# Kernel optimization log

Measured on AMD Instinct MI355X. Metric: run time of the kernel, lower is better.

## Reference

```python
import jax, jax.numpy as jnp
import numpy as np

B, S, D, H = 2, 2048, 1024, 16
HD = D // H
NEG = -1000000.0


def setup_inputs() -> dict:
    key = jax.random.key(0)
    ks = jax.random.split(key, 8)
    sc = 1.0 / np.sqrt(D)
    return {
        "q": jax.random.normal(ks[0], (B, S, D), dtype=jnp.float32),
        "k": jax.random.normal(ks[1], (B, S, D), dtype=jnp.float32),
        "v": jax.random.normal(ks[2], (B, S, D), dtype=jnp.float32),
        "valid_lens": jax.random.randint(ks[3], (B,), 1, S + 1, dtype=jnp.int32),
        "Wq": jax.random.normal(ks[4], (D, D), dtype=jnp.float32) * sc,
        "Wk": jax.random.normal(ks[5], (D, D), dtype=jnp.float32) * sc,
        "Wv": jax.random.normal(ks[6], (D, D), dtype=jnp.float32) * sc,
        "Wo": jax.random.normal(ks[7], (D, D), dtype=jnp.float32) * sc,
    }


def reference(q, k, v, valid_lens, Wq, Wk, Wv, Wo):
    # projections: [B,S,D] -> [B,H,S,HD]
    def split_heads(x):
        return x.reshape(B, S, H, HD).transpose(0, 2, 1, 3)

    qh = split_heads(q @ Wq)
    kh = split_heads(k @ Wk)
    vh = split_heads(v @ Wv)

    # scaled dot-product scores: [B,H,Sq,Sk]
    scores = jnp.einsum("bhqd,bhkd->bhqk", qh, kh) / jnp.sqrt(
        jnp.asarray(HD, dtype=jnp.float32))

    # sequence mask over key axis: positions >= valid_len replaced by -1e6
    key_pos = jnp.arange(S, dtype=jnp.int32)
    mask = key_pos[None, :] < valid_lens[:, None]            # [B,Sk]
    scores = jnp.where(mask[:, None, None, :], scores, NEG)

    attn = jax.nn.softmax(scores, axis=-1)                   # dropout rate 0
    ctx = jnp.einsum("bhqk,bhkd->bhqd", attn, vh)            # [B,H,S,HD]
    out = ctx.transpose(0, 2, 1, 3).reshape(B, S, D)
    return out @ Wo
```

## Files before the change

### kernel.cpp

```cpp
#include <hip/hip_runtime.h>
#include <math.h>

#define NB 2
#define NS 2048
#define ND 1024
#define NH 16
#define NHD 64
#define GK 1024
#define NEG -1000000.0f

typedef __attribute__((ext_vector_type(4))) float f32x4;
typedef __attribute__((ext_vector_type(8))) _Float16 f16x8;
typedef __attribute__((ext_vector_type(4))) _Float16 f16x4;

typedef const __attribute__((address_space(1))) unsigned int* gas_t;
typedef __attribute__((address_space(3))) unsigned int* las_t;

__global__ __launch_bounds__(256) void wt_kernel(const float* __restrict__ Wq,
                                                 const float* __restrict__ Wk,
                                                 const float* __restrict__ Wv,
                                                 const float* __restrict__ Wo,
                                                 _Float16* __restrict__ WtBase) {
  __shared__ _Float16 Ts[64][72];
  const int which = blockIdx.x >> 8;
  const int rem = blockIdx.x & 255;
  const int tk = rem >> 4;
  const int tn = rem & 15;
  const float* W = which == 0 ? Wq : which == 1 ? Wk : which == 2 ? Wv : Wo;
  _Float16* Wt = WtBase + (size_t)which * (GK * ND);
  const int t = threadIdx.x;
#pragma unroll
  for (int p = 0; p < 4; ++p) {
    const int kr = (p << 4) + (t >> 4);
    const int nc = (t & 15) << 2;
    float4 v = *(const float4*)(W + (size_t)((tk << 6) + kr) * ND + (tn << 6) + nc);
    f16x4 h = {(_Float16)v.x, (_Float16)v.y, (_Float16)v.z, (_Float16)v.w};
    *(f16x4*)&Ts[kr][nc] = h;
  }
  __syncthreads();
#pragma unroll
  for (int p = 0; p < 4; ++p) {
    const int nr = (p << 4) + (t >> 4);
    const int kc = (t & 15) << 2;
    f16x4 h;
#pragma unroll
    for (int u = 0; u < 4; ++u) h[u] = Ts[kc + u][nr];
    *(f16x4*)(Wt + (size_t)((tn << 6) + nr) * GK + (tk << 6) + kc) = h;
  }
}

template<int AMODE, int OMODE, int BN>
__global__ __launch_bounds__(256) void gemm_kernel(const void* __restrict__ Ap0,
                                                   const void* __restrict__ Ap1,
                                                   const void* __restrict__ Ap2,
                                                   const _Float16* __restrict__ BtBase,
                                                   void* __restrict__ OutBase) {
  constexpr int BM = 128, BK = 32;
  constexpr int NBN = ND / BN;
  constexpr int BLKS = (NB * NS / BM) * NBN;
  constexpr int NF = BN / 32;
  __shared__ float    As32[AMODE == 0 ? BM * BK : 8];
  __shared__ _Float16 As16[AMODE == 1 ? BM * BK : 8];
  __shared__ _Float16 Bs[BN * BK];

  int idx = blockIdx.x;
  const int which = idx / BLKS;
  idx -= which * BLKS;
  const int bm = (idx / NBN) * BM;
  const int bn = (idx % NBN) * BN;
  const void* Ap = which == 0 ? Ap0 : which == 1 ? Ap1 : Ap2;
  const _Float16* Bt = BtBase + (size_t)which * (ND * GK);

  const int tid = threadIdx.x, lane = tid & 63, w = tid >> 6;
  const int i16 = lane & 15, g4 = lane >> 4;
  const int wr = w >> 1, wc = w & 1;

  f32x4 acc[4][NF] = {};

  for (int kt = 0; kt < GK / BK; ++kt) {
    if (AMODE == 0) {
      const float* A = (const float*)Ap;
#pragma unroll
      for (int u = 0; u < 4; ++u) {
        const int chunk = (((w << 2) + u) << 6) + lane;
        const int r = chunk >> 3;
        const int c = (chunk & 7) ^ (r & 7);
        __builtin_amdgcn_global_load_lds(
            (gas_t)(const void*)(A + (size_t)(bm + r) * GK + (kt << 5) + (c << 2)),
            (las_t)(void*)&As32[((w << 2) + u) << 8], 16, 0, 0);
      }
    } else {
      const _Float16* A = (const _Float16*)Ap;
#pragma unroll
      for (int u = 0; u < 2; ++u) {
        const int chunk = (((w << 1) + u) << 6) + lane;
        const int r = chunk >> 2;
        const int c = (chunk & 3) ^ (r & 3);
        const int m = bm + r;
        const int kcol = (kt << 5) + (c << 3);
        const int bb = m >> 11, ss = m & (NS - 1);
        const int hh = kcol >> 6, dd = kcol & 63;
        __builtin_amdgcn_global_load_lds(
            (gas_t)(const void*)(A + (((size_t)(bb * NH + hh) * NS + ss) << 6) + dd),
            (las_t)(void*)&As16[((w << 1) + u) << 9], 16, 0, 0);
      }
    }
    {
      constexpr int CPT = (BN * BK * 2 / 16) / 256;
#pragma unroll
      for (int u = 0; u < CPT; ++u) {
        const int chunk = ((w * CPT + u) << 6) + lane;
        const int r = chunk >> 2;
        const int c = (chunk & 3) ^ (r & 3);
        __builtin_amdgcn_global_load_lds(
            (gas_t)(const void*)(Bt + (size_t)(bn + r) * GK + (kt << 5) + (c << 3)),
            (las_t)(void*)&Bs[(w * CPT + u) << 9], 16, 0, 0);
      }
    }
    __syncthreads();

    f16x8 af[4], bf[NF];
#pragma unroll
    for (int mi = 0; mi < 4; ++mi) {
      const int r = (wr << 6) + (mi << 4) + i16;
      if (AMODE == 0) {
        const f32x4 v0 = *(const f32x4*)&As32[(r << 5) + ((((g4 << 1) | 0) ^ (r & 7)) << 2)];
        const f32x4 v1 = *(const f32x4*)&As32[(r << 5) + ((((g4 << 1) | 1) ^ (r & 7)) << 2)];
        f16x8 h;
#pragma unroll
        for (int j = 0; j < 4; ++j) { h[j] = (_Float16)v0[j]; h[4 + j] = (_Float16)v1[j]; }
        af[mi] = h;
      } else {
        af[mi] = *(const f16x8*)&As16[(r << 5) + ((g4 ^ (r & 3)) << 3)];
      }
    }
#pragma unroll
    for (int ni = 0; ni < NF; ++ni) {
      const int r = wc * (BN / 2) + (ni << 4) + i16;
      bf[ni] = *(const f16x8*)&Bs[(r << 5) + ((g4 ^ (r & 3)) << 3)];
    }
#pragma unroll
    for (int mi = 0; mi < 4; ++mi)
#pragma unroll
      for (int ni = 0; ni < NF; ++ni)
        acc[mi][ni] = __builtin_amdgcn_mfma_f32_16x16x32_f16(af[mi], bf[ni], acc[mi][ni], 0, 0, 0);
    __syncthreads();
  }

#pragma unroll
  for (int mi = 0; mi < 4; ++mi)
#pragma unroll
    for (int ni = 0; ni < NF; ++ni)
#pragma unroll
      for (int j = 0; j < 4; ++j) {
        const int row = bm + (wr << 6) + (mi << 4) + (g4 << 2) + j;
        const int col = bn + wc * (BN / 2) + (ni << 4) + i16;
        const float val = acc[mi][ni][j];
        if (OMODE == 0) {
          const int bb = row >> 11, ss = row & (NS - 1);
          const int hh = col >> 6, dd = col & 63;
          _Float16* Out = (_Float16*)OutBase + (size_t)which * ((size_t)NB * NS * ND);
          Out[(((size_t)(bb * NH + hh) * NS + ss) << 6) + dd] = (_Float16)val;
        } else {
          ((float*)OutBase)[(size_t)row * ND + col] = val;
        }
      }
}

__global__ __launch_bounds__(256) void attn_kernel(_Float16* __restrict__ Qc,
                                                   const _Float16* __restrict__ Kh,
                                                   const _Float16* __restrict__ Vh,
                                                   const int* __restrict__ valid_lens) {
  __shared__ _Float16 Ks[64][72];
  __shared__ _Float16 Vt[64][72];
  __shared__ _Float16 Ps[64][72];

  const int nqt = NS >> 6;
  const int bh = blockIdx.x / nqt;
  const int qt = blockIdx.x % nqt;
  const int b = bh >> 4;
  const int valid = valid_lens[b];
  const int tid = threadIdx.x, lane = tid & 63, w = tid >> 6;
  const int i16 = lane & 15, g4 = lane >> 4;

  _Float16* Qb = Qc + ((size_t)bh * NS + (qt << 6)) * NHD;
  const _Float16* Kb = Kh + (size_t)bh * NS * NHD;
  const _Float16* Vb = Vh + (size_t)bh * NS * NHD;

  f16x8 qf[2];
#pragma unroll
  for (int dc = 0; dc < 2; ++dc)
    qf[dc] = *(const f16x8*)(Qb + (size_t)((w << 4) + i16) * NHD + (dc << 5) + (g4 << 3));

  f32x4 acc[4] = {};
  float mrow[4] = {-1e30f, -1e30f, -1e30f, -1e30f};
  float lsum[4] = {0.f, 0.f, 0.f, 0.f};

  const int ntiles = (valid + 63) >> 6;
  for (int t = 0; t < ntiles; ++t) {
    __syncthreads();
#pragma unroll
    for (int u = 0; u < 2; ++u) {
      const int chunk = (u << 8) + tid;
      const int r = chunk >> 3, c8 = (chunk & 7) << 3;
      *(f16x8*)&Ks[r][c8] = *(const f16x8*)(Kb + (size_t)((t << 6) + r) * NHD + c8);
    }
    {
      const int kv = tid >> 2;
      const int db = (tid & 3) << 4;
#pragma unroll
      for (int u = 0; u < 4; ++u) {
        f16x4 vv = *(const f16x4*)(Vb + (size_t)((t << 6) + kv) * NHD + db + (u << 2));
#pragma unroll
        for (int e = 0; e < 4; ++e) Vt[db + (u << 2) + e][kv] = vv[e];
      }
    }
    __syncthreads();

    float pj[4][4];
#pragma unroll
    for (int cf = 0; cf < 4; ++cf) {
      f32x4 sa = {};
#pragma unroll
      for (int dc = 0; dc < 2; ++dc) {
        f16x8 kf = *(const f16x8*)&Ks[(cf << 4) + i16][(dc << 5) + (g4 << 3)];
        sa = __builtin_amdgcn_mfma_f32_16x16x32_f16(qf[dc], kf, sa, 0, 0, 0);
      }
      const int kvcol = (t << 6) + (cf << 4) + i16;
#pragma unroll
      for (int j = 0; j < 4; ++j)
        pj[cf][j] = (kvcol >= valid) ? NEG : sa[j] * 0.125f;
    }

    float tmax[4];
#pragma unroll
    for (int j = 0; j < 4; ++j)
      tmax[j] = fmaxf(fmaxf(pj[0][j], pj[1][j]), fmaxf(pj[2][j], pj[3][j]));
    for (int off = 1; off < 16; off <<= 1)
#pragma unroll
      for (int j = 0; j < 4; ++j)
        tmax[j] = fmaxf(tmax[j], __shfl_xor(tmax[j], off, 64));

    float rowsum[4] = {0.f, 0.f, 0.f, 0.f};
#pragma unroll
    for (int j = 0; j < 4; ++j) {
      const float mn = fmaxf(mrow[j], tmax[j]);
      const float scv = __expf(mrow[j] - mn);
      mrow[j] = mn;
      lsum[j] *= scv;
#pragma unroll
      for (int dn = 0; dn < 4; ++dn) acc[dn][j] *= scv;
    }
#pragma unroll
    for (int cf = 0; cf < 4; ++cf)
#pragma unroll
      for (int j = 0; j < 4; ++j) {
        const float p = __expf(pj[cf][j] - mrow[j]);
        rowsum[j] += p;
        Ps[(w << 4) + (g4 << 2) + j][(cf << 4) + i16] = (_Float16)p;
      }
    for (int off = 1; off < 16; off <<= 1)
#pragma unroll
      for (int j = 0; j < 4; ++j)
        rowsum[j] += __shfl_xor(rowsum[j], off, 64);
#pragma unroll
    for (int j = 0; j < 4; ++j) lsum[j] += rowsum[j];

#pragma unroll
    for (int ks = 0; ks < 2; ++ks) {
      f16x8 pf = *(const f16x8*)&Ps[(w << 4) + i16][(ks << 5) + (g4 << 3)];
#pragma unroll
      for (int dn = 0; dn < 4; ++dn) {
        f16x8 vf = *(const f16x8*)&Vt[(dn << 4) + i16][(ks << 5) + (g4 << 3)];
        acc[dn] = __builtin_amdgcn_mfma_f32_16x16x32_f16(pf, vf, acc[dn], 0, 0, 0);
      }
    }
  }

#pragma unroll
  for (int dn = 0; dn < 4; ++dn)
#pragma unroll
    for (int j = 0; j < 4; ++j) {
      const int qrow = (w << 4) + (g4 << 2) + j;
      Qb[(size_t)qrow * NHD + (dn << 4) + i16] = (_Float16)(acc[dn][j] / lsum[j]);
    }
}

extern "C" void kernel_launch(void* const* d_in, const int* in_sizes, int n_in,
                              void* d_out, int out_size, void* d_ws, size_t ws_size,
                              hipStream_t stream) {
  const float* q  = (const float*)d_in[0];
  const float* k  = (const float*)d_in[1];
  const float* v  = (const float*)d_in[2];
  const int*   vl = (const int*)d_in[3];
  const float* Wq = (const float*)d_in[4];
  const float* Wk = (const float*)d_in[5];
  const float* Wv = (const float*)d_in[6];
  const float* Wo = (const float*)d_in[7];

  _Float16* ws = (_Float16*)d_ws;
  _Float16* Qh = ws;
  _Float16* Kh = ws + 4194304;
  _Float16* Vh = ws + 8388608;
  _Float16* Wt = ws + 12582912;

  wt_kernel<<<dim3(1024), dim3(256), 0, stream>>>(Wq, Wk, Wv, Wo, Wt);
  gemm_kernel<0, 0, 128><<<dim3(768), dim3(256), 0, stream>>>(q, k, v, Wt, Qh);
  attn_kernel<<<dim3(NB * NH * (NS >> 6)), dim3(256), 0, stream>>>(Qh, Kh, Vh, vl);
  gemm_kernel<1, 1, 64><<<dim3(512), dim3(256), 0, stream>>>(Qh, Qh, Qh, Wt + 3145728, d_out);
}
```

Before: 249.6 us.

## Restructure projection, attention and output kernels with transposed V and double buffering

The projection GEMM now converts the fp32 activations to fp16 in registers before writing LDS, so the A tile in LDS is half the size. It also folds the 1/sqrt(HD) scale into Q and writes V pre-transposed per head. Attention stages K and V^T into double-buffered LDS with async global-to-LDS loads and swizzled layouts, which removes the per-thread transpose scatter into LDS. It also skips masking on fully valid tiles and remaps block indices for cache locality. The output GEMM becomes its own specialised kernel with a remapped block order. Together these aim to cut LDS traffic and load latency, at the cost of synchronous global loads in the projection A path and a strided scatter store for the V^T output.

Measured after the change: 226.1 us. -9.4%, faster.

```diff
diff --git a/kernel.cpp b/kernel.cpp
--- a/kernel.cpp
+++ b/kernel.cpp
@@ -49,143 +49,124 @@
   }
 }
 
-template<int AMODE, int OMODE, int BN>
-__global__ __launch_bounds__(256) void gemm_kernel(const void* __restrict__ Ap0,
-                                                   const void* __restrict__ Ap1,
-                                                   const void* __restrict__ Ap2,
-                                                   const _Float16* __restrict__ BtBase,
-                                                   void* __restrict__ OutBase) {
-  constexpr int BM = 128, BK = 32;
-  constexpr int NBN = ND / BN;
-  constexpr int BLKS = (NB * NS / BM) * NBN;
-  constexpr int NF = BN / 32;
-  __shared__ float    As32[AMODE == 0 ? BM * BK : 8];
-  __shared__ _Float16 As16[AMODE == 1 ? BM * BK : 8];
-  __shared__ _Float16 Bs[BN * BK];
-
-  int idx = blockIdx.x;
-  const int which = idx / BLKS;
-  idx -= which * BLKS;
-  const int bm = (idx / NBN) * BM;
-  const int bn = (idx % NBN) * BN;
-  const void* Ap = which == 0 ? Ap0 : which == 1 ? Ap1 : Ap2;
-  const _Float16* Bt = BtBase + (size_t)which * (ND * GK);
+__global__ __launch_bounds__(256) void proj_kernel(const float* __restrict__ xq,
+                                                   const float* __restrict__ xk,
+                                                   const float* __restrict__ xv,
+                                                   const _Float16* __restrict__ WtBase,
+                                                   _Float16* __restrict__ Qh,
+                                                   _Float16* __restrict__ Kh,
+                                                   _Float16* __restrict__ VhT) {
+  constexpr int BK = 32;
+  __shared__ alignas(16) _Float16 As[128 * BK];
+  __shared__ alignas(16) _Float16 Bs[128 * BK];
+
+  int idx = ((blockIdx.x % 96) << 3) + (blockIdx.x / 96);
+  const int which = idx >> 8;
+  idx &= 255;
+  const int bm = (idx >> 3) << 7;
+  const int bn = (idx & 7) << 7;
+  const float* A = which == 0 ? xq : which == 1 ? xk : xv;
+  const _Float16* Bt = WtBase + (size_t)which * (ND * GK);
 
   const int tid = threadIdx.x, lane = tid & 63, w = tid >> 6;
   const int i16 = lane & 15, g4 = lane >> 4;
   const int wr = w >> 1, wc = w & 1;
 
-  f32x4 acc[4][NF] = {};
+  f32x4 acc[4][4] = {};
 
   for (int kt = 0; kt < GK / BK; ++kt) {
-    if (AMODE == 0) {
-      const float* A = (const float*)Ap;
-#pragma unroll
-      for (int u = 0; u < 4; ++u) {
-        const int chunk = (((w << 2) + u) << 6) + lane;
-        const int r = chunk >> 3;
-        const int c = (chunk & 7) ^ (r & 7);
-        __builtin_amdgcn_global_load_lds(
-            (gas_t)(const void*)(A + (size_t)(bm + r) * GK + (kt << 5) + (c << 2)),
-            (las_t)(void*)&As32[((w << 2) + u) << 8], 16, 0, 0);
-      }
-    } else {
-      const _Float16* A = (const _Float16*)Ap;
-#pragma unroll
-      for (int u = 0; u < 2; ++u) {
-        const int chunk = (((w << 1) + u) << 6) + lane;
-        const int r = chunk >> 2;
-        const int c = (chunk & 3) ^ (r & 3);
-        const int m = bm + r;
-        const int kcol = (kt << 5) + (c << 3);
-        const int bb = m >> 11, ss = m & (NS - 1);
-        const int hh = kcol >> 6, dd = kcol & 63;
-        __builtin_amdgcn_global_load_lds(
-            (gas_t)(const void*)(A + (((size_t)(bb * NH + hh) * NS + ss) << 6) + dd),
-            (las_t)(void*)&As16[((w << 1) + u) << 9], 16, 0, 0);
-      }
-    }
-    {
-      constexpr int CPT = (BN * BK * 2 / 16) / 256;
-#pragma unroll
-      for (int u = 0; u < CPT; ++u) {
-        const int chunk = ((w * CPT + u) << 6) + lane;
-        const int r = chunk >> 2;
-        const int c = (chunk & 3) ^ (r & 3);
-        __builtin_amdgcn_global_load_lds(
-            (gas_t)(const void*)(Bt + (size_t)(bn + r) * GK + (kt << 5) + (c << 3)),
-            (las_t)(void*)&Bs[(w * CPT + u) << 9], 16, 0, 0);
-      }
-    }
-    __syncthreads();
-
-    f16x8 af[4], bf[NF];
+#pragma unroll
+    for (int u = 0; u < 2; ++u) {
+      const int c = (((w << 1) + u) << 6) + lane;
+      const int r = c >> 2, sl = c & 3;
+      const float* src = A + (size_t)(bm + r) * GK + (kt << 5) + ((sl ^ (r & 3)) << 3);
+      float4 v0 = *(const float4*)src;
+      float4 v1 = *(const float4*)(src + 4);
+      f16x8 h;
+#pragma unroll
+      for (int j = 0; j < 4; ++j) { h[j] = (_Float16)v0[j]; h[4 + j] = (_Float16)v1[j]; }
+      *(f16x8*)&As[(r << 5) + (sl << 3)] = h;
+    }
+#pragma unroll
+    for (int u = 0; u < 2; ++u) {
+      const int cb = ((w << 1) + u) << 6;
+      const int c = cb + lane;
+      const int r = c >> 2, sl = c & 3;
+      __builtin_amdgcn_global_load_lds(
+          (gas_t)(const void*)(Bt + (size_t)(bn + r) * GK + (kt << 5) + ((sl ^ (r & 3)) << 3)),
+          (las_t)(void*)&Bs[cb << 3], 16, 0, 0);
+    }
+    __syncthreads();
+
+    f16x8 af[4], bf[4];
 #pragma unroll
     for (int mi = 0; mi < 4; ++mi) {
       const int r = (wr << 6) + (mi << 4) + i16;
-      if (AMODE == 0) {
-        const f32x4 v0 = *(const f32x4*)&As32[(r << 5) + ((((g4 << 1) | 0) ^ (r & 7)) << 2)];
-        const f32x4 v1 = *(const f32x4*)&As32[(r << 5) + ((((g4 << 1) | 1) ^ (r & 7)) << 2)];
-        f16x8 h;
-#pragma unroll
-        for (int j = 0; j < 4; ++j) { h[j] = (_Float16)v0[j]; h[4 + j] = (_Float16)v1[j]; }
-        af[mi] = h;
-      } else {
-        af[mi] = *(const f16x8*)&As16[(r << 5) + ((g4 ^ (r & 3)) << 3)];
-      }
-    }
-#pragma unroll
-    for (int ni = 0; ni < NF; ++ni) {
-      const int r = wc * (BN / 2) + (ni << 4) + i16;
+      af[mi] = *(const f16x8*)&As[(r << 5) + ((g4 ^ (r & 3)) << 3)];
+    }
+#pragma unroll
+    for (int ni = 0; ni < 4; ++ni) {
+      const int r = (wc << 6) + (ni << 4) + i16;
       bf[ni] = *(const f16x8*)&Bs[(r << 5) + ((g4 ^ (r & 3)) << 3)];
     }
 #pragma unroll
     for (int mi = 0; mi < 4; ++mi)
 #pragma unroll
-      for (int ni = 0; ni < NF; ++ni)
+      for (int ni = 0; ni < 4; ++ni)
         acc[mi][ni] = __builtin_amdgcn_mfma_f32_16x16x32_f16(af[mi], bf[ni], acc[mi][ni], 0, 0, 0);
     __syncthreads();
   }
 
-#pragma unroll
-  for (int mi = 0; mi < 4; ++mi)
-#pragma unroll
-    for (int ni = 0; ni < NF; ++ni)
-#pragma unroll
-      for (int j = 0; j < 4; ++j) {
-        const int row = bm + (wr << 6) + (mi << 4) + (g4 << 2) + j;
-        const int col = bn + wc * (BN / 2) + (ni << 4) + i16;
-        const float val = acc[mi][ni][j];
-        if (OMODE == 0) {
+  if (which == 2) {
+#pragma unroll
+    for (int mi = 0; mi < 4; ++mi)
+#pragma unroll
+      for (int ni = 0; ni < 4; ++ni) {
+        const int row0 = bm + (wr << 6) + (mi << 4) + (g4 << 2);
+        const int col = bn + (wc << 6) + (ni << 4) + i16;
+        const int bb = row0 >> 11, ss = row0 & (NS - 1);
+        const int hh = col >> 6, dd = col & 63;
+        f16x4 hv;
+#pragma unroll
+        for (int j = 0; j < 4; ++j) hv[j] = (_Float16)acc[mi][ni][j];
+        *(f16x4*)&VhT[(((size_t)(bb * NH + hh) * NHD + dd) << 11) + ss] = hv;
+      }
+  } else {
+    const float scale = which == 0 ? 0.125f : 1.0f;
+    _Float16* Out = which == 0 ? Qh : Kh;
+#pragma unroll
+    for (int mi = 0; mi < 4; ++mi)
+#pragma unroll
+      for (int ni = 0; ni < 4; ++ni)
+#pragma unroll
+        for (int j = 0; j < 4; ++j) {
+          const int row = bm + (wr << 6) + (mi << 4) + (g4 << 2) + j;
+          const int col = bn + (wc << 6) + (ni << 4) + i16;
           const int bb = row >> 11, ss = row & (NS - 1);
           const int hh = col >> 6, dd = col & 63;
-          _Float16* Out = (_Float16*)OutBase + (size_t)which * ((size_t)NB * NS * ND);
-          Out[(((size_t)(bb * NH + hh) * NS + ss) << 6) + dd] = (_Float16)val;
-        } else {
-          ((float*)OutBase)[(size_t)row * ND + col] = val;
+          Out[(((size_t)(bb * NH + hh) * NS + ss) << 6) + dd] = (_Float16)(acc[mi][ni][j] * scale);
         }
-      }
+  }
 }
 
 __global__ __launch_bounds__(256) void attn_kernel(_Float16* __restrict__ Qc,
                                                    const _Float16* __restrict__ Kh,
-                                                   const _Float16* __restrict__ Vh,
+                                                   const _Float16* __restrict__ VhT,
                                                    const int* __restrict__ valid_lens) {
-  __shared__ _Float16 Ks[64][72];
-  __shared__ _Float16 Vt[64][72];
-  __shared__ _Float16 Ps[64][72];
-
-  const int nqt = NS >> 6;
-  const int bh = blockIdx.x / nqt;
-  const int qt = blockIdx.x % nqt;
-  const int b = bh >> 4;
-  const int valid = valid_lens[b];
+  __shared__ alignas(16) _Float16 Ks[2][4096];
+  __shared__ alignas(16) _Float16 Vt[2][4096];
+  __shared__ alignas(16) _Float16 Ps[64][72];
+
+  const int b0 = blockIdx.x;
+  const int idx = ((b0 & 7) << 5) + ((b0 >> 8) << 8) + ((b0 >> 3) & 31);
+  const int bh = idx >> 5, qt = idx & 31;
+  const int valid = valid_lens[bh >> 4];
   const int tid = threadIdx.x, lane = tid & 63, w = tid >> 6;
   const int i16 = lane & 15, g4 = lane >> 4;
 
   _Float16* Qb = Qc + ((size_t)bh * NS + (qt << 6)) * NHD;
   const _Float16* Kb = Kh + (size_t)bh * NS * NHD;
-  const _Float16* Vb = Vh + (size_t)bh * NS * NHD;
+  const _Float16* Vb = VhT + (size_t)bh * NHD * NS;
 
   f16x8 qf[2];
 #pragma unroll
@@ -196,40 +177,49 @@
   float mrow[4] = {-1e30f, -1e30f, -1e30f, -1e30f};
   float lsum[4] = {0.f, 0.f, 0.f, 0.f};
 
+  auto STAGE = [&](int buf, int t) {
+#pragma unroll
+    for (int u = 0; u < 2; ++u) {
+      const int cb = ((w << 1) + u) << 6;
+      const int c = cb + lane;
+      const int r = c >> 3, sl = c & 7;
+      const int so = (sl ^ (r & 7)) << 3;
+      __builtin_amdgcn_global_load_lds(
+          (gas_t)(const void*)(Kb + (size_t)((t << 6) + r) * NHD + so),
+          (las_t)(void*)&Ks[buf][cb << 3], 16, 0, 0);
+      __builtin_amdgcn_global_load_lds(
+          (gas_t)(const void*)(Vb + (size_t)r * NS + (t << 6) + so),
+          (las_t)(void*)&Vt[buf][cb << 3], 16, 0, 0);
+    }
+  };
+
   const int ntiles = (valid + 63) >> 6;
+  STAGE(0, 0);
+
   for (int t = 0; t < ntiles; ++t) {
     __syncthreads();
-#pragma unroll
-    for (int u = 0; u < 2; ++u) {
-      const int chunk = (u << 8) + tid;
-      const int r = chunk >> 3, c8 = (chunk & 7) << 3;
-      *(f16x8*)&Ks[r][c8] = *(const f16x8*)(Kb + (size_t)((t << 6) + r) * NHD + c8);
-    }
-    {
-      const int kv = tid >> 2;
-      const int db = (tid & 3) << 4;
-#pragma unroll
-      for (int u = 0; u < 4; ++u) {
-        f16x4 vv = *(const f16x4*)(Vb + (size_t)((t << 6) + kv) * NHD + db + (u << 2));
-#pragma unroll
-        for (int e = 0; e < 4; ++e) Vt[db + (u << 2) + e][kv] = vv[e];
-      }
-    }
-    __syncthreads();
+    if (t + 1 < ntiles) STAGE((t + 1) & 1, t + 1);
+    const int buf = t & 1;
+    const bool full = ((t + 1) << 6) <= valid;
 
     float pj[4][4];
 #pragma unroll
     for (int cf = 0; cf < 4; ++cf) {
       f32x4 sa = {};
+      const int r = (cf << 4) + i16;
 #pragma unroll
       for (int dc = 0; dc < 2; ++dc) {
-        f16x8 kf = *(const f16x8*)&Ks[(cf << 4) + i16][(dc << 5) + (g4 << 3)];
+        f16x8 kf = *(const f16x8*)&Ks[buf][(r << 6) + ((((dc << 2) + g4) ^ (r & 7)) << 3)];
         sa = __builtin_amdgcn_mfma_f32_16x16x32_f16(qf[dc], kf, sa, 0, 0, 0);
       }
-      const int kvcol = (t << 6) + (cf << 4) + i16;
-#pragma unroll
-      for (int j = 0; j < 4; ++j)
-        pj[cf][j] = (kvcol >= valid) ? NEG : sa[j] * 0.125f;
+      if (full) {
+#pragma unroll
+        for (int j = 0; j < 4; ++j) pj[cf][j] = sa[j];
+      } else {
+        const int kvcol = (t << 6) + r;
+#pragma unroll
+        for (int j = 0; j < 4; ++j) pj[cf][j] = (kvcol >= valid) ? NEG : sa[j];
+      }
     }
 
     float tmax[4];
@@ -271,7 +261,8 @@
       f16x8 pf = *(const f16x8*)&Ps[(w << 4) + i16][(ks << 5) + (g4 << 3)];
 #pragma unroll
       for (int dn = 0; dn < 4; ++dn) {
-        f16x8 vf = *(const f16x8*)&Vt[(dn << 4) + i16][(ks << 5) + (g4 << 3)];
+        const int d = (dn << 4) + i16;
+        f16x8 vf = *(const f16x8*)&Vt[buf][(d << 6) + ((((ks << 2) + g4) ^ (d & 7)) << 3)];
         acc[dn] = __builtin_amdgcn_mfma_f32_16x16x32_f16(pf, vf, acc[dn], 0, 0, 0);
       }
     }
@@ -284,6 +275,78 @@
       const int qrow = (w << 4) + (g4 << 2) + j;
       Qb[(size_t)qrow * NHD + (dn << 4) + i16] = (_Float16)(acc[dn][j] / lsum[j]);
     }
+}
+
+__global__ __launch_bounds__(256) void out_kernel(const _Float16* __restrict__ ctx,
+                                                  const _Float16* __restrict__ Wot,
+                                                  float* __restrict__ Out) {
+  constexpr int BK = 32;
+  __shared__ alignas(16) _Float16 As[128 * BK];
+  __shared__ alignas(16) _Float16 Bs[64 * BK];
+
+  const int idx = ((blockIdx.x % 64) << 3) + (blockIdx.x / 64);
+  const int bm = (idx >> 4) << 7;
+  const int bn = (idx & 15) << 6;
+
+  const int tid = threadIdx.x, lane = tid & 63, w = tid >> 6;
+  const int i16 = lane & 15, g4 = lane >> 4;
+  const int wr = w >> 1, wc = w & 1;
+
+  f32x4 acc[4][2] = {};
+
+  for (int kt = 0; kt < GK / BK; ++kt) {
+#pragma unroll
+    for (int u = 0; u < 2; ++u) {
+      const int cb = ((w << 1) + u) << 6;
+      const int c = cb + lane;
+      const int r = c >> 2, sl = c & 3;
+      const int m = bm + r;
+      const int kcol = (kt << 5) + ((sl ^ (r & 3)) << 3);
+      const int bb = m >> 11, ss = m & (NS - 1);
+      const int hh = kcol >> 6, dd = kcol & 63;
+      __builtin_amdgcn_global_load_lds(
+          (gas_t)(const void*)(ctx + (((size_t)(bb * NH + hh) * NS + ss) << 6) + dd),
+          (las_t)(void*)&As[cb << 3], 16, 0, 0);
+    }
+    {
+      const int cb = w << 6;
+      const int c = cb + lane;
+      const int r = c >> 2, sl = c & 3;
+      __builtin_amdgcn_global_load_lds(
+          (gas_t)(const void*)(Wot + (size_t)(bn + r) * GK + (kt << 5) + ((sl ^ (r & 3)) << 3)),
+          (las_t)(void*)&Bs[cb << 3], 16, 0, 0);
+    }
+    __syncthreads();
+
+    f16x8 af[4], bf[2];
+#pragma unroll
+    for (int mi = 0; mi < 4; ++mi) {
+      const int r = (wr << 6) + (mi << 4) + i16;
+      af[mi] = *(const f16x8*)&As[(r << 5) + ((g4 ^ (r & 3)) << 3)];
+    }
+#pragma unroll
+    for (int ni = 0; ni < 2; ++ni) {
+      const int r = (wc << 5) + (ni << 4) + i16;
+      bf[ni] = *(const f16x8*)&Bs[(r << 5) + ((g4 ^ (r & 3)) << 3)];
+    }
+#pragma unroll
+    for (int mi = 0; mi < 4; ++mi)
+#pragma unroll
+      for (int ni = 0; ni < 2; ++ni)
+        acc[mi][ni] = __builtin_amdgcn_mfma_f32_16x16x32_f16(af[mi], bf[ni], acc[mi][ni], 0, 0, 0);
+    __syncthreads();
+  }
+
+#pragma unroll
+  for (int mi = 0; mi < 4; ++mi)
+#pragma unroll
+    for (int ni = 0; ni < 2; ++ni)
+#pragma unroll
+      for (int j = 0; j < 4; ++j) {
+        const int row = bm + (wr << 6) + (mi << 4) + (g4 << 2) + j;
+        const int col = bn + (wc << 5) + (ni << 4) + i16;
+        Out[(size_t)row * ND + col] = acc[mi][ni][j];
+      }
 }
 
 extern "C" void kernel_launch(void* const* d_in, const int* in_sizes, int n_in,
@@ -299,13 +362,13 @@
   const float* Wo = (const float*)d_in[7];
 
   _Float16* ws = (_Float16*)d_ws;
-  _Float16* Qh = ws;
-  _Float16* Kh = ws + 4194304;
-  _Float16* Vh = ws + 8388608;
-  _Float16* Wt = ws + 12582912;
+  _Float16* Qh  = ws;
+  _Float16* Kh  = ws + 4194304;
+  _Float16* VhT = ws + 8388608;
+  _Float16* Wt  = ws + 12582912;
 
   wt_kernel<<<dim3(1024), dim3(256), 0, stream>>>(Wq, Wk, Wv, Wo, Wt);
-  gemm_kernel<0, 0, 128><<<dim3(768), dim3(256), 0, stream>>>(q, k, v, Wt, Qh);
-  attn_kernel<<<dim3(NB * NH * (NS >> 6)), dim3(256), 0, stream>>>(Qh, Kh, Vh, vl);
-  gemm_kernel<1, 1, 64><<<dim3(512), dim3(256), 0, stream>>>(Qh, Qh, Qh, Wt + 3145728, d_out);
-}
+  proj_kernel<<<dim3(768), dim3(256), 0, stream>>>(q, k, v, Wt, Qh, Kh, VhT);
+  attn_kernel<<<dim3(NB * NH * (NS >> 6)), dim3(256), 0, stream>>>(Qh, Kh, VhT, vl);
+  out_kernel<<<dim3(512), dim3(256), 0, stream>>>(Qh, Wt + 3145728, (float*)d_out);
+}
```
